# Performance work log

Hardware: AMD Instinct MI355X
Metric: run time of the kernel (lower is better)

The kernel has to match this reference:

```python
import jax, jax.numpy as jnp
import numpy as np

N_QKV = 64
N_EMBED = 2048
B = 4
T = 2048  # must equal N_EMBED because the module's causal mask is n_embed x n_embed


def setup_inputs() -> dict:
    key = jax.random.key(0)
    ks = jax.random.split(key, 7)
    s = 1.0 / np.sqrt(N_EMBED)
    return {
        "x": jax.random.normal(ks[0], (B, T, N_EMBED), dtype=jnp.float32),
        "Wq": jax.random.normal(ks[1], (N_QKV, N_EMBED), dtype=jnp.float32) * s,
        "bq": jnp.zeros((N_QKV,), dtype=jnp.float32),
        "Wk": jax.random.normal(ks[2], (N_QKV, N_EMBED), dtype=jnp.float32) * s,
        "bk": jnp.zeros((N_QKV,), dtype=jnp.float32),
        "Wv": jax.random.normal(ks[3], (N_QKV, N_EMBED), dtype=jnp.float32) * s,
        "bv": jnp.zeros((N_QKV,), dtype=jnp.float32),
    }


def reference(x, Wq, bq, Wk, bk, Wv, bv):
    # Linear projections: torch nn.Linear computes x @ W.T + b
    q = jnp.einsum("bte,qe->btq", x, Wq) + bq  # [B, T, n_qkv]
    k = jnp.einsum("bte,qe->btq", x, Wk) + bk
    v = jnp.einsum("bte,qe->btq", x, Wv) + bv
    scale = 1.0 / jnp.sqrt(jnp.asarray(N_QKV, dtype=x.dtype))
    logits = jnp.einsum("btq,bsq->bts", q, k) * scale  # [B, T, T]
    # causal mask: upper triangle (strictly above diagonal) -> -inf
    causal = jnp.tril(jnp.ones((T, T), dtype=bool))
    logits = jnp.where(causal, logits, jnp.asarray(-jnp.inf, dtype=logits.dtype))
    probs = jax.nn.softmax(logits, axis=-1)
    return jnp.einsum("bts,bsq->btq", probs, v)  # [B, T, n_qkv]
```

## Files before the change

kernel.cpp:

```cpp
#include <hip/hip_runtime.h>
#include <hip/hip_bf16.h>

#define T_SEQ 2048
#define E_DIM 2048
#define D_HEAD 64
#define B_SZ 4
#define NROWS (B_SZ * T_SEQ)

typedef __attribute__((ext_vector_type(8))) short bf16x8;
typedef __attribute__((ext_vector_type(4))) float f32x4;
typedef __attribute__((ext_vector_type(4))) unsigned short u16x4;
typedef __attribute__((ext_vector_type(8))) unsigned short u16x8;

__device__ __forceinline__ unsigned short f2bf(float x) {
    __hip_bfloat16 h = __float2bfloat16(x);
    return *reinterpret_cast<unsigned short*>(&h);
}

__device__ __forceinline__ u16x8 cvt8(float4 a, float4 b) {
    u16x8 t;
    t[0] = f2bf(a.x); t[1] = f2bf(a.y); t[2] = f2bf(a.z); t[3] = f2bf(a.w);
    t[4] = f2bf(b.x); t[5] = f2bf(b.y); t[6] = f2bf(b.z); t[7] = f2bf(b.w);
    return t;
}

__device__ __forceinline__ bf16x8 cvtfrag2(f32x4 lo, f32x4 hi) {
    bf16x8 f;
    #pragma unroll
    for (int j = 0; j < 4; ++j) {
        f[j]     = (short)f2bf(lo[j]);
        f[4 + j] = (short)f2bf(hi[j]);
    }
    return f;
}

__device__ __forceinline__ bf16x8 ldfrag(const unsigned short* p) {
    u16x4 lo = *(const u16x4*)p;
    u16x4 hi = *(const u16x4*)(p + 16);
    bf16x8 f;
    #pragma unroll
    for (int j = 0; j < 4; ++j) { f[j] = (short)lo[j]; f[4 + j] = (short)hi[j]; }
    return f;
}

__device__ __forceinline__ void lds_fence_barrier() {
    asm volatile("s_waitcnt lgkmcnt(0)" ::: "memory");
    __builtin_amdgcn_s_barrier();
}

__device__ __forceinline__ void gl_lds16(const void* gsrc, void* ldst) {
    __builtin_amdgcn_global_load_lds(
        (const __attribute__((address_space(1))) unsigned int*)(unsigned long long)gsrc,
        (__attribute__((address_space(3))) unsigned int*)(unsigned long long)ldst,
        16, 0, 0);
}

__global__ __launch_bounds__(256) void wcvt_kernel(
    const float* __restrict__ Wq, const float* __restrict__ Wk,
    const float* __restrict__ Wv, unsigned short* __restrict__ Wp)
{
    const int gid = blockIdx.x * 256 + threadIdx.x;
    const int l    = gid & 63;
    const int k32  = (gid >> 6) & 63;
    const int f    = gid >> 12;
    const int r    = l & 15;
    const int g    = l >> 4;
    const int n    = 16 * f + r;
    const int pj   = n >> 6;
    const int o    = n & 63;
    const float* __restrict__ src = (pj == 0) ? Wq : (pj == 1) ? Wk : Wv;
    const float* p = src + (size_t)o * E_DIM + k32 * 32 + g * 4;
    float4 a = *(const float4*)p;
    float4 b = *(const float4*)(p + 16);
    *(u16x8*)(Wp + (size_t)gid * 8) = cvt8(a, b);
}

__global__ __launch_bounds__(256, 2) void proj_mfma_kernel(
    const float* __restrict__ x, const unsigned short* __restrict__ Wp,
    const float* __restrict__ bq, const float* __restrict__ bk,
    const float* __restrict__ bv,
    __hip_bfloat16* __restrict__ qb, __hip_bfloat16* __restrict__ kb,
    __hip_bfloat16* __restrict__ vb)
{
    __shared__ unsigned char lds[2][28672];

    const int tid  = threadIdx.x;
    const int wn   = tid >> 6;
    const int l    = tid & 63;
    const int r    = l & 15;
    const int g    = l >> 4;
    const int row0 = blockIdx.x * 16;

    const int xrow = tid >> 4;
    const int xjl  = (tid & 15) ^ (xrow & 7);
    const unsigned char* xsrc =
        (const unsigned char*)(x + (size_t)(row0 + xrow) * E_DIM + xjl * 4);
    const int xdst = tid * 16;
    const unsigned char* wsrc[6];
    int wdst[6];
    #pragma unroll
    for (int i = 0; i < 6; ++i) {
        const int cw = tid + i * 256;
        const int f  = cw >> 7;
        const int kc = (cw >> 6) & 1;
        const int lw = cw & 63;
        wsrc[i] = (const unsigned char*)Wp + (size_t)(f * 64 + kc) * 1024 + lw * 16;
        wdst[i] = 4096 + cw * 16;
    }

    f32x4 acc[3];
    #pragma unroll
    for (int ff = 0; ff < 3; ++ff) acc[ff] = (f32x4){0.f, 0.f, 0.f, 0.f};

    auto stage = [&](int t, int bi) {
        gl_lds16(xsrc + (size_t)t * 256, &lds[bi][xdst]);
        #pragma unroll
        for (int i = 0; i < 6; ++i)
            gl_lds16(wsrc[i] + (size_t)t * 2048, &lds[bi][wdst[i]]);
    };

    const int amask = r & 7;
    const int abase = r * 256;

    auto compute = [&](int bi) {
        bf16x8 af[2];
        #pragma unroll
        for (int kk = 0; kk < 2; ++kk) {
            f32x4 lo = *(const f32x4*)&lds[bi][abase + (((kk * 8 + g)     ^ amask) * 16)];
            f32x4 hi = *(const f32x4*)&lds[bi][abase + (((kk * 8 + 4 + g) ^ amask) * 16)];
            af[kk] = cvtfrag2(lo, hi);
        }
        #pragma unroll
        for (int ff = 0; ff < 3; ++ff) {
            const int f = wn * 3 + ff;
            #pragma unroll
            for (int kk = 0; kk < 2; ++kk) {
                bf16x8 bfm = *(const bf16x8*)&lds[bi][4096 + ((f * 2 + kk) * 64 + l) * 16];
                acc[ff] = __builtin_amdgcn_mfma_f32_16x16x32_bf16(af[kk], bfm, acc[ff], 0, 0, 0);
            }
        }
    };

    stage(0, 0);
    asm volatile("s_waitcnt vmcnt(0)" ::: "memory");
    __builtin_amdgcn_s_barrier();

    for (int t = 0; t < 32; ++t) {
        if (t < 31) stage(t + 1, (t + 1) & 1);
        compute(t & 1);
        asm volatile("s_waitcnt vmcnt(0)" ::: "memory");
        __builtin_amdgcn_s_barrier();
    }

    #pragma unroll
    for (int ff = 0; ff < 3; ++ff) {
        const int f  = wn * 3 + ff;
        const int n  = 16 * f + r;
        const int pj = n >> 6;
        const int o  = n & 63;
        const float* bias = (pj == 0) ? bq : (pj == 1) ? bk : bv;
        __hip_bfloat16* dst = (pj == 0) ? qb : (pj == 1) ? kb : vb;
        const float scale = (pj == 0) ? 0.18033688011112042f : 1.0f;
        const float bv_ = bias[o];
        #pragma unroll
        for (int j = 0; j < 4; ++j) {
            const int row = row0 + 4 * g + j;
            dst[(size_t)row * D_HEAD + o] =
                __float2bfloat16((acc[ff][j] + bv_) * scale);
        }
    }
}

#define LDK 72
#define LDV 68
#define LDP 68

__global__ __launch_bounds__(128) void attn_part_kernel(
    const __hip_bfloat16* __restrict__ qg, const __hip_bfloat16* __restrict__ kg,
    const __hip_bfloat16* __restrict__ vg, float* __restrict__ Op,
    float* __restrict__ Ml, int tpc, int nch)
{
    const int qt = blockIdx.x;
    const int ch = blockIdx.y;
    const int total64 = qt / 2 + 1;
    if (ch * tpc >= total64) return;

    __shared__ unsigned short Kl[64 * LDK];
    __shared__ unsigned short Vt[64 * LDV];
    __shared__ unsigned short Pl[2 * 16 * LDP];

    const int tid = threadIdx.x;
    const int w   = tid >> 6;
    const int l   = tid & 63;
    const int r   = l & 15;
    const int g   = l >> 4;
    const int q0  = qt * 32;
    const int b   = blockIdx.z;
    const size_t base = (size_t)b * T_SEQ;

    const unsigned short* qb16 = (const unsigned short*)qg;
    const unsigned short* kb16 = (const unsigned short*)kg;
    const unsigned short* vb16 = (const unsigned short*)vg;

    const unsigned short* qrow = qb16 + (base + q0 + 16 * w + r) * D_HEAD;
    bf16x8 qf[2];
    #pragma unroll
    for (int kk = 0; kk < 2; ++kk)
        qf[kk] = ldfrag(qrow + 32 * kk + 4 * g);

    f32x4 acc_o[4];
    #pragma unroll
    for (int dn = 0; dn < 4; ++dn) acc_o[dn] = (f32x4){0.f, 0.f, 0.f, 0.f};
    float m4[4] = {-1e30f, -1e30f, -1e30f, -1e30f};
    float l4[4] = {0.f, 0.f, 0.f, 0.f};

    unsigned short* pw = &Pl[w * 16 * LDP];
    const int ntiles = min(tpc, total64 - ch * tpc);
    const int y = tid & 15, z = tid >> 4;
    const int s0base = ch * tpc * 64;

    u16x8 kr[4];
    u16x4 va4[4], vb4[4];

    auto issue = [&](int s0) {
        #pragma unroll
        for (int i = 0; i < 4; ++i) {
            const int c = tid + i * 128;
            kr[i] = *(const u16x8*)(kb16 + (base + s0 + (c >> 3)) * D_HEAD + (c & 7) * 8);
        }
        #pragma unroll
        for (int m = 0; m < 4; ++m) {
            const int sl = 2 * (z + 8 * m);
            const int d0 = y * 4;
            va4[m] = *(const u16x4*)(vb16 + (base + s0 + sl) * D_HEAD + d0);
            vb4[m] = *(const u16x4*)(vb16 + (base + s0 + sl + 1) * D_HEAD + d0);
        }
    };

    issue(s0base);

    for (int it = 0; it < ntiles; ++it) {
        const int s0 = s0base + it * 64;

        __builtin_amdgcn_s_barrier();

        #pragma unroll
        for (int i = 0; i < 4; ++i) {
            const int c = tid + i * 128;
            *(u16x8*)(&Kl[(c >> 3) * LDK + (c & 7) * 8]) = kr[i];
        }
        #pragma unroll
        for (int m = 0; m < 4; ++m) {
            const int sl = 2 * (z + 8 * m);
            const int d0 = y * 4;
            #pragma unroll
            for (int i = 0; i < 4; ++i) {
                unsigned int pr = (unsigned int)(unsigned short)va4[m][i] |
                                  ((unsigned int)(unsigned short)vb4[m][i] << 16);
                *(unsigned int*)&Vt[(d0 + i) * LDV + sl] = pr;
            }
        }
        lds_fence_barrier();

        if (it + 1 < ntiles) issue(s0 + 64);

        f32x4 s_acc[4];
        #pragma unroll
        for (int nt = 0; nt < 4; ++nt) s_acc[nt] = (f32x4){0.f, 0.f, 0.f, 0.f};
        #pragma unroll
        for (int nt = 0; nt < 4; ++nt)
            #pragma unroll
            for (int kk = 0; kk < 2; ++kk) {
                bf16x8 bf = ldfrag(&Kl[(nt * 16 + r) * LDK + kk * 32 + 4 * g]);
                s_acc[nt] = __builtin_amdgcn_mfma_f32_16x16x32_bf16(qf[kk], bf, s_acc[nt], 0, 0, 0);
            }

        if (s0 + 64 > q0) {
            #pragma unroll
            for (int nt = 0; nt < 4; ++nt)
                #pragma unroll
                for (int j = 0; j < 4; ++j)
                    if (s0 + nt * 16 + r > q0 + 16 * w + 4 * g + j)
                        s_acc[nt][j] = -1e30f;
        }

        float tm[4];
        #pragma unroll
        for (int j = 0; j < 4; ++j)
            tm[j] = fmaxf(fmaxf(s_acc[0][j], s_acc[1][j]),
                          fmaxf(s_acc[2][j], s_acc[3][j]));
        #pragma unroll
        for (int mask = 1; mask < 16; mask <<= 1)
            #pragma unroll
            for (int j = 0; j < 4; ++j)
                tm[j] = fmaxf(tm[j], __shfl_xor(tm[j], mask));

        float p[4][4], rs[4];
        #pragma unroll
        for (int j = 0; j < 4; ++j) {
            const float mn = fmaxf(m4[j], tm[j]);
            const float sc = exp2f(m4[j] - mn);
            m4[j] = mn;
            rs[j] = 0.f;
            #pragma unroll
            for (int nt = 0; nt < 4; ++nt) {
                p[nt][j] = exp2f(s_acc[nt][j] - mn);
                rs[j] += p[nt][j];
            }
            l4[j] *= sc;
            acc_o[0][j] *= sc; acc_o[1][j] *= sc;
            acc_o[2][j] *= sc; acc_o[3][j] *= sc;
        }
        #pragma unroll
        for (int mask = 1; mask < 16; mask <<= 1)
            #pragma unroll
            for (int j = 0; j < 4; ++j)
                rs[j] += __shfl_xor(rs[j], mask);
        #pragma unroll
        for (int j = 0; j < 4; ++j) l4[j] += rs[j];

        #pragma unroll
        for (int nt = 0; nt < 4; ++nt)
            #pragma unroll
            for (int j = 0; j < 4; ++j)
                pw[(4 * g + j) * LDP + nt * 16 + r] = f2bf(p[nt][j]);

        bf16x8 pf[2];
        #pragma unroll
        for (int kk = 0; kk < 2; ++kk)
            pf[kk] = ldfrag(&pw[r * LDP + kk * 32 + 4 * g]);

        #pragma unroll
        for (int dn = 0; dn < 4; ++dn)
            #pragma unroll
            for (int kk = 0; kk < 2; ++kk) {
                bf16x8 vf = ldfrag(&Vt[(dn * 16 + r) * LDV + kk * 32 + 4 * g]);
                acc_o[dn] = __builtin_amdgcn_mfma_f32_16x16x32_bf16(pf[kk], vf, acc_o[dn], 0, 0, 0);
            }
    }

    const size_t pidx = ((size_t)(b * 64 + qt) * nch + ch);
    float* op = Op + pidx * 2048;
    #pragma unroll
    for (int j = 0; j < 4; ++j) {
        const int row = 16 * w + 4 * g + j;
        #pragma unroll
        for (int dn = 0; dn < 4; ++dn)
            op[row * 64 + dn * 16 + r] = acc_o[dn][j];
        if (r == 0) {
            Ml[pidx * 64 + row]      = m4[j];
            Ml[pidx * 64 + 32 + row] = l4[j];
        }
    }
}

__global__ __launch_bounds__(256) void attn_combine_kernel(
    const float* __restrict__ Op, const float* __restrict__ Ml,
    float* __restrict__ out, int tpc, int nch)
{
    const int qt = blockIdx.x;
    const int b  = blockIdx.y;
    const int total64 = qt / 2 + 1;
    const int nact = (total64 + tpc - 1) / tpc;
    const size_t pbase = (size_t)(b * 64 + qt) * nch;

    __shared__ float wgt[8][32];
    __shared__ float linv[32];

    const int tid = threadIdx.x;
    if (tid < 32) {
        float M = -1e30f;
        for (int c = 0; c < nact; ++c)
            M = fmaxf(M, Ml[(pbase + c) * 64 + tid]);
        float L = 0.f;
        for (int c = 0; c < nact; ++c) {
            float wv = exp2f(Ml[(pbase + c) * 64 + tid] - M);
            wgt[c][tid] = wv;
            L += wv * Ml[(pbase + c) * 64 + 32 + tid];
        }
        linv[tid] = 1.0f / L;
    }
    __syncthreads();

    const int d  = tid & 63;
    const int r0 = tid >> 6;
    for (int row = r0; row < 32; row += 4) {
        float a = 0.f;
        for (int c = 0; c < nact; ++c)
            a += wgt[c][row] * Op[(pbase + c) * 2048 + row * 64 + d];
        out[((size_t)b * T_SEQ + qt * 32 + row) * D_HEAD + d] = a * linv[row];
    }
}

extern "C" void kernel_launch(void* const* d_in, const int* in_sizes, int n_in,
                              void* d_out, int out_size, void* d_ws, size_t ws_size,
                              hipStream_t stream) {
    const float* x  = (const float*)d_in[0];
    const float* Wq = (const float*)d_in[1];
    const float* bq = (const float*)d_in[2];
    const float* Wk = (const float*)d_in[3];
    const float* bk = (const float*)d_in[4];
    const float* Wv = (const float*)d_in[5];
    const float* bv = (const float*)d_in[6];
    float* out = (float*)d_out;

    __hip_bfloat16* qb = (__hip_bfloat16*)d_ws;
    __hip_bfloat16* kb = qb + (size_t)NROWS * D_HEAD;
    __hip_bfloat16* vb = kb + (size_t)NROWS * D_HEAD;
    unsigned short* Wp = (unsigned short*)(vb + (size_t)NROWS * D_HEAD);
    float* Op = (float*)((char*)d_ws + (4u << 20));

    int nch = 8;
    while (nch > 1 &&
           (4u << 20) + (size_t)256 * nch * (2048 + 64) * 4 > ws_size)
        nch >>= 1;
    const int tpc = 32 / nch;
    float* Ml = Op + (size_t)256 * nch * 2048;

    wcvt_kernel<<<192, 256, 0, stream>>>(Wq, Wk, Wv, Wp);
    proj_mfma_kernel<<<NROWS / 16, 256, 0, stream>>>(x, Wp, bq, bk, bv, qb, kb, vb);
    attn_part_kernel<<<dim3(64, nch, B_SZ), 128, 0, stream>>>(qb, kb, vb, Op, Ml, tpc, nch);
    attn_combine_kernel<<<dim3(64, B_SZ), 256, 0, stream>>>(Op, Ml, out, tpc, nch);
}
```

Baseline: 69.14 us.

## Split projection GEMM along K with direct global loads and separate reduction kernel

The QKV projection now splits the 2048-wide reduction into two halves across twice as many blocks, which are loaded directly from global memory into registers instead of staged through double-buffered LDS. The partial fp32 sums go to workspace and a new finalize kernel adds them, applies bias and scale, and writes bf16 q/k/v. The aim is more parallelism and occupancy, with no LDS barriers, for a memory-bound projection. In exchange it costs an extra kernel launch and an fp32 partial-buffer round trip, and it weakens the workspace size check used to choose nch.

```diff
diff --git a/kernel.cpp b/kernel.cpp
--- a/kernel.cpp
+++ b/kernel.cpp
@@ -46,13 +46,6 @@
 __device__ __forceinline__ void lds_fence_barrier() {
     asm volatile("s_waitcnt lgkmcnt(0)" ::: "memory");
     __builtin_amdgcn_s_barrier();
-}
-
-__device__ __forceinline__ void gl_lds16(const void* gsrc, void* ldst) {
-    __builtin_amdgcn_global_load_lds(
-        (const __attribute__((address_space(1))) unsigned int*)(unsigned long long)gsrc,
-        (__attribute__((address_space(3))) unsigned int*)(unsigned long long)ldst,
-        16, 0, 0);
 }
 
 __global__ __launch_bounds__(256) void wcvt_kernel(
@@ -75,100 +68,80 @@
     *(u16x8*)(Wp + (size_t)gid * 8) = cvt8(a, b);
 }
 
-__global__ __launch_bounds__(256, 2) void proj_mfma_kernel(
+__global__ __launch_bounds__(256, 4) void proj_part_kernel(
     const float* __restrict__ x, const unsigned short* __restrict__ Wp,
+    float* __restrict__ Cpart)
+{
+    const int tid = threadIdx.x;
+    const int wn  = tid >> 6;
+    const int l   = tid & 63;
+    const int r   = l & 15;
+    const int g   = l >> 4;
+    const int ks  = blockIdx.x & 1;
+    const int rt  = blockIdx.x >> 1;
+    const int row0 = rt * 16;
+
+    const float* xrow = x + (size_t)(row0 + r) * E_DIM + ks * 1024 + 4 * g;
+    const unsigned char* wpb = (const unsigned char*)Wp + l * 16;
+
+    f32x4 acc[3];
+    #pragma unroll
+    for (int ff = 0; ff < 3; ++ff) acc[ff] = (f32x4){0.f, 0.f, 0.f, 0.f};
+
+    #pragma unroll 4
+    for (int t = 0; t < 16; ++t) {
+        bf16x8 af[2];
+        #pragma unroll
+        for (int kk = 0; kk < 2; ++kk) {
+            f32x4 lo = *(const f32x4*)(xrow + t * 64 + kk * 32);
+            f32x4 hi = *(const f32x4*)(xrow + t * 64 + kk * 32 + 16);
+            af[kk] = cvtfrag2(lo, hi);
+        }
+        #pragma unroll
+        for (int ff = 0; ff < 3; ++ff) {
+            const int f = wn * 3 + ff;
+            #pragma unroll
+            for (int kk = 0; kk < 2; ++kk) {
+                bf16x8 bfm = *(const bf16x8*)(
+                    wpb + (size_t)(f * 64 + ks * 32 + 2 * t + kk) * 1024);
+                acc[ff] = __builtin_amdgcn_mfma_f32_16x16x32_bf16(
+                    af[kk], bfm, acc[ff], 0, 0, 0);
+            }
+        }
+    }
+
+    float* cp = Cpart + (size_t)ks * NROWS * 192;
+    #pragma unroll
+    for (int ff = 0; ff < 3; ++ff) {
+        const int n = 16 * (wn * 3 + ff) + r;
+        #pragma unroll
+        for (int j = 0; j < 4; ++j)
+            cp[(size_t)(row0 + 4 * g + j) * 192 + n] = acc[ff][j];
+    }
+}
+
+__global__ __launch_bounds__(256) void proj_fin_kernel(
+    const float* __restrict__ Cpart,
     const float* __restrict__ bq, const float* __restrict__ bk,
     const float* __restrict__ bv,
     __hip_bfloat16* __restrict__ qb, __hip_bfloat16* __restrict__ kb,
     __hip_bfloat16* __restrict__ vb)
 {
-    __shared__ unsigned char lds[2][28672];
-
-    const int tid  = threadIdx.x;
-    const int wn   = tid >> 6;
-    const int l    = tid & 63;
-    const int r    = l & 15;
-    const int g    = l >> 4;
-    const int row0 = blockIdx.x * 16;
-
-    const int xrow = tid >> 4;
-    const int xjl  = (tid & 15) ^ (xrow & 7);
-    const unsigned char* xsrc =
-        (const unsigned char*)(x + (size_t)(row0 + xrow) * E_DIM + xjl * 4);
-    const int xdst = tid * 16;
-    const unsigned char* wsrc[6];
-    int wdst[6];
-    #pragma unroll
-    for (int i = 0; i < 6; ++i) {
-        const int cw = tid + i * 256;
-        const int f  = cw >> 7;
-        const int kc = (cw >> 6) & 1;
-        const int lw = cw & 63;
-        wsrc[i] = (const unsigned char*)Wp + (size_t)(f * 64 + kc) * 1024 + lw * 16;
-        wdst[i] = 4096 + cw * 16;
-    }
-
-    f32x4 acc[3];
-    #pragma unroll
-    for (int ff = 0; ff < 3; ++ff) acc[ff] = (f32x4){0.f, 0.f, 0.f, 0.f};
-
-    auto stage = [&](int t, int bi) {
-        gl_lds16(xsrc + (size_t)t * 256, &lds[bi][xdst]);
-        #pragma unroll
-        for (int i = 0; i < 6; ++i)
-            gl_lds16(wsrc[i] + (size_t)t * 2048, &lds[bi][wdst[i]]);
-    };
-
-    const int amask = r & 7;
-    const int abase = r * 256;
-
-    auto compute = [&](int bi) {
-        bf16x8 af[2];
-        #pragma unroll
-        for (int kk = 0; kk < 2; ++kk) {
-            f32x4 lo = *(const f32x4*)&lds[bi][abase + (((kk * 8 + g)     ^ amask) * 16)];
-            f32x4 hi = *(const f32x4*)&lds[bi][abase + (((kk * 8 + 4 + g) ^ amask) * 16)];
-            af[kk] = cvtfrag2(lo, hi);
-        }
-        #pragma unroll
-        for (int ff = 0; ff < 3; ++ff) {
-            const int f = wn * 3 + ff;
-            #pragma unroll
-            for (int kk = 0; kk < 2; ++kk) {
-                bf16x8 bfm = *(const bf16x8*)&lds[bi][4096 + ((f * 2 + kk) * 64 + l) * 16];
-                acc[ff] = __builtin_amdgcn_mfma_f32_16x16x32_bf16(af[kk], bfm, acc[ff], 0, 0, 0);
-            }
-        }
-    };
-
-    stage(0, 0);
-    asm volatile("s_waitcnt vmcnt(0)" ::: "memory");
-    __builtin_amdgcn_s_barrier();
-
-    for (int t = 0; t < 32; ++t) {
-        if (t < 31) stage(t + 1, (t + 1) & 1);
-        compute(t & 1);
-        asm volatile("s_waitcnt vmcnt(0)" ::: "memory");
-        __builtin_amdgcn_s_barrier();
-    }
-
-    #pragma unroll
-    for (int ff = 0; ff < 3; ++ff) {
-        const int f  = wn * 3 + ff;
-        const int n  = 16 * f + r;
-        const int pj = n >> 6;
-        const int o  = n & 63;
-        const float* bias = (pj == 0) ? bq : (pj == 1) ? bk : bv;
-        __hip_bfloat16* dst = (pj == 0) ? qb : (pj == 1) ? kb : vb;
-        const float scale = (pj == 0) ? 0.18033688011112042f : 1.0f;
-        const float bv_ = bias[o];
-        #pragma unroll
-        for (int j = 0; j < 4; ++j) {
-            const int row = row0 + 4 * g + j;
-            dst[(size_t)row * D_HEAD + o] =
-                __float2bfloat16((acc[ff][j] + bv_) * scale);
-        }
-    }
+    const int gid = blockIdx.x * 256 + threadIdx.x;
+    const int row = gid / 48;
+    const int n0  = (gid % 48) * 4;
+    const int pj  = n0 >> 6;
+    const int o   = n0 & 63;
+    f32x4 a = *(const f32x4*)(Cpart + (size_t)row * 192 + n0);
+    f32x4 b = *(const f32x4*)(Cpart + (size_t)NROWS * 192 + (size_t)row * 192 + n0);
+    const float* bias = (pj == 0) ? bq : (pj == 1) ? bk : bv;
+    __hip_bfloat16* dst = (pj == 0) ? qb : (pj == 1) ? kb : vb;
+    const float scale = (pj == 0) ? 0.18033688011112042f : 1.0f;
+    u16x4 outv;
+    #pragma unroll
+    for (int j = 0; j < 4; ++j)
+        outv[j] = f2bf((a[j] + b[j] + bias[o + j]) * scale);
+    *(u16x4*)((unsigned short*)dst + (size_t)row * D_HEAD + o) = outv;
 }
 
 #define LDK 72
@@ -409,16 +382,18 @@
     __hip_bfloat16* vb = kb + (size_t)NROWS * D_HEAD;
     unsigned short* Wp = (unsigned short*)(vb + (size_t)NROWS * D_HEAD);
     float* Op = (float*)((char*)d_ws + (4u << 20));
+    float* Cpart = (float*)((char*)d_ws + (24u << 20));
 
     int nch = 8;
     while (nch > 1 &&
-           (4u << 20) + (size_t)256 * nch * (2048 + 64) * 4 > ws_size)
+           (24u << 20) + (size_t)2 * NROWS * 192 * 4 > ws_size)
         nch >>= 1;
     const int tpc = 32 / nch;
     float* Ml = Op + (size_t)256 * nch * 2048;
 
     wcvt_kernel<<<192, 256, 0, stream>>>(Wq, Wk, Wv, Wp);
-    proj_mfma_kernel<<<NROWS / 16, 256, 0, stream>>>(x, Wp, bq, bk, bv, qb, kb, vb);
+    proj_part_kernel<<<1024, 256, 0, stream>>>(x, Wp, Cpart);
+    proj_fin_kernel<<<NROWS * 48 / 256, 256, 0, stream>>>(Cpart, bq, bk, bv, qb, kb, vb);
     attn_part_kernel<<<dim3(64, nch, B_SZ), 128, 0, stream>>>(qb, kb, vb, Op, Ml, tpc, nch);
     attn_combine_kernel<<<dim3(64, B_SZ), 256, 0, stream>>>(Op, Ml, out, tpc, nch);
 }
```

Measured after the change: 93.87 us. 1.36x slower.
